# Optimization experiments

Measured on AMD Instinct MI355X. Metric: run time of the kernel, lower is better.

Reference implementation:

```python
import jax, jax.numpy as jnp
import numpy as np

NEG_SLOPE = 0.2

def setup_inputs() -> dict:
    key = jax.random.key(0)
    k1, k2, k3 = jax.random.split(key, 3)
    N, d, attn = 1024, 256, 256
    H = jax.random.normal(k1, (N, d), dtype=jnp.float32)
    # nn.Linear(2*d, attn, bias=False).weight has shape [attn, 2*d]
    W = jax.random.normal(k2, (attn, 2 * d), dtype=jnp.float32) * 0.05
    a = jax.random.normal(k3, (attn, 1), dtype=jnp.float32) * 0.05
    return {"H": H, "W": W, "a": a}

def reference(H, W, a):
    # Faithful to: E = leakyrelu(Linear(cat[H_i, H_j])); scores = E @ a; alpha = softmax(scores, dim=1); out = alpha @ H
    # Decompose W into halves acting on H_i and H_j to avoid the N x N x 2d concat:
    d = H.shape[1]
    W1, W2 = W[:, :d], W[:, d:]          # each [attn, d]
    Wh1 = H @ W1.T                        # [N, attn] (contribution of H_i)
    Wh2 = H @ W2.T                        # [N, attn] (contribution of H_j)
    E = jax.nn.leaky_relu(Wh1[:, None, :] + Wh2[None, :, :], NEG_SLOPE)  # [N, N, attn]
    scores = jnp.einsum('ijk,ko->ij', E, a)   # [N, N]
    alpha = jax.nn.softmax(scores, axis=1)    # softmax over j (dim=1)
    return alpha @ H                          # [N, d] weighted sum of H_j
```

## Files before the change

kernel.cpp:

```cpp
#include <hip/hip_runtime.h>


#define HALF 524288

#define FENCE_BAR() do {                                   \
    __builtin_amdgcn_sched_barrier(0);                     \
    asm volatile("s_waitcnt lgkmcnt(0)" ::: "memory");     \
    __builtin_amdgcn_s_barrier();                          \
    __builtin_amdgcn_sched_barrier(0);                     \
} while (0)

__global__ __launch_bounds__(256) void k1_gemm_wh(const float* __restrict__ H,
                                                  const float* __restrict__ W,
                                                  float* __restrict__ Whp) {
    __shared__ float As[64][36];
    __shared__ float Bs[32][36];
    const int bi = blockIdx.x, bm = blockIdx.y, bz = blockIdx.z;
    const int t = threadIdx.x;
    const int ti = t >> 4, tj = t & 15;
    const int i0 = ti * 4;
    const int half = bm >> 3;
    const int kbase = bz * 128;
    float acc[4][2] = {};
    for (int kc = 0; kc < 128; kc += 32) {
        const int kg = kbase + kc;
        {
            const int r = t >> 2, c = (t & 3) * 8;
            *(float4*)&As[r][c] = *(const float4*)&H[(bi * 64 + r) * 256 + kg + c];
            *(float4*)&As[r][c + 4] =
                *(const float4*)&H[(bi * 64 + r) * 256 + kg + c + 4];
        }
        {
            const int r = t >> 3, c = (t & 7) * 4;
            const int wrow = (bm * 32 + r) & 255;
            *(float4*)&Bs[r][c] =
                *(const float4*)&W[wrow * 512 + half * 256 + kg + c];
        }
        __syncthreads();
#pragma unroll
        for (int k = 0; k < 32; k += 4) {
            float4 a[4], b[2];
#pragma unroll
            for (int r = 0; r < 4; ++r) a[r] = *(const float4*)&As[i0 + r][k];
#pragma unroll
            for (int c = 0; c < 2; ++c) b[c] = *(const float4*)&Bs[tj + 16 * c][k];
#pragma unroll
            for (int r = 0; r < 4; ++r)
#pragma unroll
                for (int c = 0; c < 2; ++c) {
                    acc[r][c] = fmaf(a[r].x, b[c].x, acc[r][c]);
                    acc[r][c] = fmaf(a[r].y, b[c].y, acc[r][c]);
                    acc[r][c] = fmaf(a[r].z, b[c].z, acc[r][c]);
                    acc[r][c] = fmaf(a[r].w, b[c].w, acc[r][c]);
                }
        }
        __syncthreads();
    }
    float* dst = Whp + (size_t)bz * HALF;
#pragma unroll
    for (int r = 0; r < 4; ++r)
#pragma unroll
        for (int c = 0; c < 2; ++c)
            dst[(size_t)(bi * 64 + i0 + r) * 512 + bm * 32 + tj + 16 * c] = acc[r][c];
}

__global__ __launch_bounds__(256) void kW_merge(const float* __restrict__ Whp,
                                                const float* __restrict__ a,
                                                float* __restrict__ Wh,
                                                float* __restrict__ s2) {
    const int t = threadIdx.x;
    const int row = blockIdx.x * 2 + (t >> 7);
    const int col = (t & 127) * 4;
    const size_t off = (size_t)row * 512 + col;
    float4 v0 = *(const float4*)&Whp[off];
    float4 v1 = *(const float4*)&Whp[HALF + off];
    float4 v = make_float4(v0.x + v1.x, v0.y + v1.y, v0.z + v1.z, v0.w + v1.w);
    *(float4*)&Wh[off] = v;
    if (col >= 256) {
        float4 av = *(const float4*)&a[col - 256];
        float p = av.x * v.x + av.y * v.y + av.z * v.z + av.w * v.w;
#pragma unroll
        for (int o = 32; o > 0; o >>= 1) p += __shfl_xor(p, o);
        if ((t & 63) == 0) s2[row] = 0.6f * p;
    }
}

__global__ __launch_bounds__(256) void kF_flash(const float* __restrict__ Wh,
                                                const float* __restrict__ a,
                                                const float* __restrict__ s2,
                                                const float* __restrict__ H,
                                                float* __restrict__ avp,
                                                float* __restrict__ mbuf,
                                                float* __restrict__ lbuf) {
    __shared__ float SH[16640];
    __shared__ float P[32 * 68];
    __shared__ float bsh[256];
    float* X1 = SH;
    float* X2 = SH + 4352;
    float* Hs = SH;
    const int bi = blockIdx.x, bj = blockIdx.y;
    const int t = threadIdx.x;
    const int ti = t >> 4, tj = t & 15;
    const int i0 = ti * 2;
    const int r1 = t >> 3, c1 = (t & 7) * 8;
    const int r2 = t >> 2, c2 = (t & 3) * 16;
    const float* g1 = Wh + (size_t)(bi * 32 + r1) * 512 + c1;
    const float* g2 = Wh + (size_t)(bj * 64 + r2) * 512 + 256 + c2;
    const int hr = t >> 2, hc = (t & 3) * 64;
    const float* gH = H + (size_t)(bj * 64 + hr) * 256 + hc;

    float4 A0, A1, A2, A3, A4, A5, B0, B1, B2, B3, B4, B5;

#define LOADC_A(mc) do { A0 = *(const float4*)(g1 + (mc)*64); \
    A1 = *(const float4*)(g1 + (mc)*64 + 4);                  \
    A2 = *(const float4*)(g2 + (mc)*64);                      \
    A3 = *(const float4*)(g2 + (mc)*64 + 4);                  \
    A4 = *(const float4*)(g2 + (mc)*64 + 8);                  \
    A5 = *(const float4*)(g2 + (mc)*64 + 12); } while (0)
#define LOADC_B(mc) do { B0 = *(const float4*)(g1 + (mc)*64); \
    B1 = *(const float4*)(g1 + (mc)*64 + 4);                  \
    B2 = *(const float4*)(g2 + (mc)*64);                      \
    B3 = *(const float4*)(g2 + (mc)*64 + 4);                  \
    B4 = *(const float4*)(g2 + (mc)*64 + 8);                  \
    B5 = *(const float4*)(g2 + (mc)*64 + 12); } while (0)
#define WRITEC_A(buf) do {                                    \
    *(float4*)&X1[((buf) * 32 + r1) * 68 + c1] = A0;          \
    *(float4*)&X1[((buf) * 32 + r1) * 68 + c1 + 4] = A1;      \
    *(float4*)&X2[((buf) * 64 + r2) * 68 + c2] = A2;          \
    *(float4*)&X2[((buf) * 64 + r2) * 68 + c2 + 4] = A3;      \
    *(float4*)&X2[((buf) * 64 + r2) * 68 + c2 + 8] = A4;      \
    *(float4*)&X2[((buf) * 64 + r2) * 68 + c2 + 12] = A5; } while (0)
#define WRITEC_B(buf) do {                                    \
    *(float4*)&X1[((buf) * 32 + r1) * 68 + c1] = B0;          \
    *(float4*)&X1[((buf) * 32 + r1) * 68 + c1 + 4] = B1;      \
    *(float4*)&X2[((buf) * 64 + r2) * 68 + c2] = B2;          \
    *(float4*)&X2[((buf) * 64 + r2) * 68 + c2 + 4] = B3;      \
    *(float4*)&X2[((buf) * 64 + r2) * 68 + c2 + 8] = B4;      \
    *(float4*)&X2[((buf) * 64 + r2) * 68 + c2 + 12] = B5; } while (0)

    LOADC_A(0);
    float s2v0 = s2[bj * 64 + tj];
    float s2v1 = s2[bj * 64 + tj + 16];
    float s2v2 = s2[bj * 64 + tj + 32];
    float s2v3 = s2[bj * 64 + tj + 48];
    if (t < 64) {
        float4 av = *(const float4*)&a[t * 4];
        *(float4*)&bsh[t * 4] =
            make_float4(0.4f * av.x, 0.4f * av.y, 0.4f * av.z, 0.4f * av.w);
    }

    float acc[2][4] = {};
#pragma unroll
    for (int mc = 0; mc < 4; ++mc) {
        const int buf = mc & 1;
        if (mc < 3) {
            if (buf == 0) LOADC_B(mc + 1); else LOADC_A(mc + 1);
        }
        if (buf == 0) WRITEC_A(0); else WRITEC_B(1);
        FENCE_BAR();
#pragma unroll
        for (int k = 0; k < 64; k += 4) {
            float4 x1[2], x2[4];
#pragma unroll
            for (int r = 0; r < 2; ++r)
                x1[r] = *(const float4*)&X1[(buf * 32 + i0 + r) * 68 + k];
#pragma unroll
            for (int c = 0; c < 4; ++c)
                x2[c] = *(const float4*)&X2[(buf * 64 + tj + 16 * c) * 68 + k];
            const float4 bv = *(const float4*)&bsh[mc * 64 + k];
#pragma unroll
            for (int r = 0; r < 2; ++r)
#pragma unroll
                for (int c = 0; c < 4; ++c) {
                    acc[r][c] = fmaf(fabsf(x1[r].x + x2[c].x), bv.x, acc[r][c]);
                    acc[r][c] = fmaf(fabsf(x1[r].y + x2[c].y), bv.y, acc[r][c]);
                    acc[r][c] = fmaf(fabsf(x1[r].z + x2[c].z), bv.z, acc[r][c]);
                    acc[r][c] = fmaf(fabsf(x1[r].w + x2[c].w), bv.w, acc[r][c]);
                }
        }
        FENCE_BAR();
    }

    acc[0][0] += s2v0; acc[1][0] += s2v0;
    acc[0][1] += s2v1; acc[1][1] += s2v1;
    acc[0][2] += s2v2; acc[1][2] += s2v2;
    acc[0][3] += s2v3; acc[1][3] += s2v3;

    float4 h0 = *(const float4*)(gH);
    float4 h1 = *(const float4*)(gH + 4);
    float4 h2 = *(const float4*)(gH + 8);
    float4 h3 = *(const float4*)(gH + 12);
    float4 h4 = *(const float4*)(gH + 16);
    float4 h5 = *(const float4*)(gH + 20);
    float4 h6 = *(const float4*)(gH + 24);
    float4 h7 = *(const float4*)(gH + 28);

    float mm0, mm1, l00, l01;
#pragma unroll
    for (int r = 0; r < 2; ++r) {
        float mm = fmaxf(fmaxf(acc[r][0], acc[r][1]), fmaxf(acc[r][2], acc[r][3]));
        mm = fmaxf(mm, __shfl_xor(mm, 1));
        mm = fmaxf(mm, __shfl_xor(mm, 2));
        mm = fmaxf(mm, __shfl_xor(mm, 4));
        mm = fmaxf(mm, __shfl_xor(mm, 8));
        float l0 = 0.f;
#pragma unroll
        for (int c = 0; c < 4; ++c) {
            acc[r][c] = __expf(acc[r][c] - mm);
            l0 += acc[r][c];
        }
        l0 += __shfl_xor(l0, 1);
        l0 += __shfl_xor(l0, 2);
        l0 += __shfl_xor(l0, 4);
        l0 += __shfl_xor(l0, 8);
#pragma unroll
        for (int c = 0; c < 4; ++c) P[(i0 + r) * 68 + tj + 16 * c] = acc[r][c];
        if (r == 0) { mm0 = mm; l00 = l0; } else { mm1 = mm; l01 = l0; }
    }
    FENCE_BAR();

    *(float4*)&Hs[hr * 260 + hc] = h0;
    *(float4*)&Hs[hr * 260 + hc + 4] = h1;
    *(float4*)&Hs[hr * 260 + hc + 8] = h2;
    *(float4*)&Hs[hr * 260 + hc + 12] = h3;
    *(float4*)&Hs[hr * 260 + hc + 16] = h4;
    *(float4*)&Hs[hr * 260 + hc + 20] = h5;
    *(float4*)&Hs[hr * 260 + hc + 24] = h6;
    *(float4*)&Hs[hr * 260 + hc + 28] = h7;
    h0 = *(const float4*)(gH + 32);
    h1 = *(const float4*)(gH + 36);
    h2 = *(const float4*)(gH + 40);
    h3 = *(const float4*)(gH + 44);
    h4 = *(const float4*)(gH + 48);
    h5 = *(const float4*)(gH + 52);
    h6 = *(const float4*)(gH + 56);
    h7 = *(const float4*)(gH + 60);
    *(float4*)&Hs[hr * 260 + hc + 32] = h0;
    *(float4*)&Hs[hr * 260 + hc + 36] = h1;
    *(float4*)&Hs[hr * 260 + hc + 40] = h2;
    *(float4*)&Hs[hr * 260 + hc + 44] = h3;
    *(float4*)&Hs[hr * 260 + hc + 48] = h4;
    *(float4*)&Hs[hr * 260 + hc + 52] = h5;
    *(float4*)&Hs[hr * 260 + hc + 56] = h6;
    *(float4*)&Hs[hr * 260 + hc + 60] = h7;
    FENCE_BAR();

    const int ti2 = t >> 5, tj2 = t & 31;
    const int ip = ti2 * 4;
    const int ca = tj2 * 4, cb = 128 + tj2 * 4;
    float4 acc2[4][2] = {};
#pragma unroll
    for (int jj = 0; jj < 64; jj += 4) {
        float4 pv[4];
#pragma unroll
        for (int r = 0; r < 4; ++r) pv[r] = *(const float4*)&P[(ip + r) * 68 + jj];
#pragma unroll
        for (int q = 0; q < 4; ++q) {
            float4 ha = *(const float4*)&Hs[(jj + q) * 260 + ca];
            float4 hb = *(const float4*)&Hs[(jj + q) * 260 + cb];
#pragma unroll
            for (int r = 0; r < 4; ++r) {
                const float s = (q == 0) ? pv[r].x : (q == 1) ? pv[r].y
                              : (q == 2) ? pv[r].z : pv[r].w;
                acc2[r][0].x = fmaf(s, ha.x, acc2[r][0].x);
                acc2[r][0].y = fmaf(s, ha.y, acc2[r][0].y);
                acc2[r][0].z = fmaf(s, ha.z, acc2[r][0].z);
                acc2[r][0].w = fmaf(s, ha.w, acc2[r][0].w);
                acc2[r][1].x = fmaf(s, hb.x, acc2[r][1].x);
                acc2[r][1].y = fmaf(s, hb.y, acc2[r][1].y);
                acc2[r][1].z = fmaf(s, hb.z, acc2[r][1].z);
                acc2[r][1].w = fmaf(s, hb.w, acc2[r][1].w);
            }
        }
    }
#pragma unroll
    for (int r = 0; r < 4; ++r) {
        const size_t o = (size_t)bj * 262144 + (size_t)(bi * 32 + ip + r) * 256;
        *(float4*)&avp[o + ca] = acc2[r][0];
        *(float4*)&avp[o + cb] = acc2[r][1];
    }
    if (tj == 0) {
        const int gi = bi * 32 + i0;
        mbuf[bj * 1024 + gi] = mm0;
        lbuf[bj * 1024 + gi] = l00;
        mbuf[bj * 1024 + gi + 1] = mm1;
        lbuf[bj * 1024 + gi + 1] = l01;
    }
#undef LOADC_A
#undef LOADC_B
#undef WRITEC_A
#undef WRITEC_B
}

__global__ __launch_bounds__(256) void kM_merge(const float* __restrict__ avp,
                                                const float* __restrict__ mbuf,
                                                const float* __restrict__ lbuf,
                                                float* __restrict__ out) {
    const int t = threadIdx.x;
    const int i = blockIdx.x * 4 + (t >> 6);
    const int c0 = (t & 63) * 4;
    float ms[16], es[16];
    float M = -1e30f;
#pragma unroll
    for (int s = 0; s < 16; ++s) {
        ms[s] = mbuf[s * 1024 + i];
        M = fmaxf(M, ms[s]);
    }
    float L = 0.f;
#pragma unroll
    for (int s = 0; s < 16; ++s) {
        es[s] = __expf(ms[s] - M);
        L = fmaf(es[s], lbuf[s * 1024 + i], L);
    }
    const float inv = 1.0f / L;
    float4 o = make_float4(0.f, 0.f, 0.f, 0.f);
#pragma unroll
    for (int s = 0; s < 16; ++s) {
        float4 p = *(const float4*)&avp[(size_t)s * 262144 + (size_t)i * 256 + c0];
        o.x = fmaf(es[s], p.x, o.x);
        o.y = fmaf(es[s], p.y, o.y);
        o.z = fmaf(es[s], p.z, o.z);
        o.w = fmaf(es[s], p.w, o.w);
    }
    o.x *= inv; o.y *= inv; o.z *= inv; o.w *= inv;
    *(float4*)&out[(size_t)i * 256 + c0] = o;
}

extern "C" void kernel_launch(void* const* d_in, const int* in_sizes, int n_in,
                              void* d_out, int out_size, void* d_ws, size_t ws_size,
                              hipStream_t stream) {
    const float* H = (const float*)d_in[0];
    const float* W = (const float*)d_in[1];
    const float* a = (const float*)d_in[2];
    float* out = (float*)d_out;
    float* ws = (float*)d_ws;

    float* avp = ws;
    float* Whp = ws;
    float* Wh = ws + (4u << 20);
    float* mbuf = Wh + HALF;
    float* lbuf = mbuf + 16384;
    float* s2 = lbuf + 16384;

    hipLaunchKernelGGL(k1_gemm_wh, dim3(16, 16, 2), dim3(256), 0, stream, H, W, Whp);
    hipLaunchKernelGGL(kW_merge, dim3(512), dim3(256), 0, stream, Whp, a, Wh, s2);
    hipLaunchKernelGGL(kF_flash, dim3(32, 16), dim3(256), 0, stream, Wh, a, s2, H,
                       avp, mbuf, lbuf);
    hipLaunchKernelGGL(kM_merge, dim3(256), dim3(256), 0, stream, avp, mbuf, lbuf, out);
}
```

Measured before the change: 49.29 us.

## Halve flash block size, double per-thread tile, prefetch two chunks ahead

The flash kernel now runs 128 threads per block instead of 256 over the same 32x64 tile, so each thread computes 4x4 scores and 8 output rows of the P@H product. Register-staged loads of Wh chunks move to a prefetch-two-ahead scheme. The pre-scaled attention vector is written to global memory once by the merge kernel rather than rebuilt in shared memory by every block. The aim is more register-level reuse per LDS load and less per-block overhead, at the cost of higher register pressure (h[32], acc2[8][2], A/B[12]), which could spill or cut occupancy.

```diff
diff --git a/kernel.cpp b/kernel.cpp
--- a/kernel.cpp
+++ b/kernel.cpp
@@ -9,6 +9,13 @@
     __builtin_amdgcn_s_barrier();                          \
     __builtin_amdgcn_sched_barrier(0);                     \
 } while (0)
+
+__device__ __forceinline__ void f4fma(float4& acc, float s, float4 h) {
+    acc.x = fmaf(s, h.x, acc.x);
+    acc.y = fmaf(s, h.y, acc.y);
+    acc.z = fmaf(s, h.z, acc.z);
+    acc.w = fmaf(s, h.w, acc.w);
+}
 
 __global__ __launch_bounds__(256) void k1_gemm_wh(const float* __restrict__ H,
                                                   const float* __restrict__ W,
@@ -67,7 +74,8 @@
 __global__ __launch_bounds__(256) void kW_merge(const float* __restrict__ Whp,
                                                 const float* __restrict__ a,
                                                 float* __restrict__ Wh,
-                                                float* __restrict__ s2) {
+                                                float* __restrict__ s2,
+                                                float* __restrict__ bglob) {
     const int t = threadIdx.x;
     const int row = blockIdx.x * 2 + (t >> 7);
     const int col = (t & 127) * 4;
@@ -83,93 +91,93 @@
         for (int o = 32; o > 0; o >>= 1) p += __shfl_xor(p, o);
         if ((t & 63) == 0) s2[row] = 0.6f * p;
     }
-}
-
-__global__ __launch_bounds__(256) void kF_flash(const float* __restrict__ Wh,
-                                                const float* __restrict__ a,
+    if (blockIdx.x == 0 && t < 64) {
+        float4 av = *(const float4*)&a[t * 4];
+        *(float4*)&bglob[t * 4] =
+            make_float4(0.4f * av.x, 0.4f * av.y, 0.4f * av.z, 0.4f * av.w);
+    }
+}
+
+__global__ __launch_bounds__(128) void kF_flash(const float* __restrict__ Wh,
+                                                const float* __restrict__ bglob,
                                                 const float* __restrict__ s2,
                                                 const float* __restrict__ H,
                                                 float* __restrict__ avp,
                                                 float* __restrict__ mbuf,
                                                 float* __restrict__ lbuf) {
     __shared__ float SH[16640];
-    __shared__ float P[32 * 68];
-    __shared__ float bsh[256];
+    __shared__ float P[2176];
     float* X1 = SH;
     float* X2 = SH + 4352;
     float* Hs = SH;
     const int bi = blockIdx.x, bj = blockIdx.y;
     const int t = threadIdx.x;
     const int ti = t >> 4, tj = t & 15;
-    const int i0 = ti * 2;
-    const int r1 = t >> 3, c1 = (t & 7) * 8;
-    const int r2 = t >> 2, c2 = (t & 3) * 16;
+    const int i0 = ti * 4;
+    const int r1 = t >> 2, c1 = (t & 3) * 16;
+    const int r2 = t >> 1, c2 = (t & 1) * 32;
     const float* g1 = Wh + (size_t)(bi * 32 + r1) * 512 + c1;
     const float* g2 = Wh + (size_t)(bj * 64 + r2) * 512 + 256 + c2;
-    const int hr = t >> 2, hc = (t & 3) * 64;
-    const float* gH = H + (size_t)(bj * 64 + hr) * 256 + hc;
-
-    float4 A0, A1, A2, A3, A4, A5, B0, B1, B2, B3, B4, B5;
-
-#define LOADC_A(mc) do { A0 = *(const float4*)(g1 + (mc)*64); \
-    A1 = *(const float4*)(g1 + (mc)*64 + 4);                  \
-    A2 = *(const float4*)(g2 + (mc)*64);                      \
-    A3 = *(const float4*)(g2 + (mc)*64 + 4);                  \
-    A4 = *(const float4*)(g2 + (mc)*64 + 8);                  \
-    A5 = *(const float4*)(g2 + (mc)*64 + 12); } while (0)
-#define LOADC_B(mc) do { B0 = *(const float4*)(g1 + (mc)*64); \
-    B1 = *(const float4*)(g1 + (mc)*64 + 4);                  \
-    B2 = *(const float4*)(g2 + (mc)*64);                      \
-    B3 = *(const float4*)(g2 + (mc)*64 + 4);                  \
-    B4 = *(const float4*)(g2 + (mc)*64 + 8);                  \
-    B5 = *(const float4*)(g2 + (mc)*64 + 12); } while (0)
-#define WRITEC_A(buf) do {                                    \
-    *(float4*)&X1[((buf) * 32 + r1) * 68 + c1] = A0;          \
-    *(float4*)&X1[((buf) * 32 + r1) * 68 + c1 + 4] = A1;      \
-    *(float4*)&X2[((buf) * 64 + r2) * 68 + c2] = A2;          \
-    *(float4*)&X2[((buf) * 64 + r2) * 68 + c2 + 4] = A3;      \
-    *(float4*)&X2[((buf) * 64 + r2) * 68 + c2 + 8] = A4;      \
-    *(float4*)&X2[((buf) * 64 + r2) * 68 + c2 + 12] = A5; } while (0)
-#define WRITEC_B(buf) do {                                    \
-    *(float4*)&X1[((buf) * 32 + r1) * 68 + c1] = B0;          \
-    *(float4*)&X1[((buf) * 32 + r1) * 68 + c1 + 4] = B1;      \
-    *(float4*)&X2[((buf) * 64 + r2) * 68 + c2] = B2;          \
-    *(float4*)&X2[((buf) * 64 + r2) * 68 + c2 + 4] = B3;      \
-    *(float4*)&X2[((buf) * 64 + r2) * 68 + c2 + 8] = B4;      \
-    *(float4*)&X2[((buf) * 64 + r2) * 68 + c2 + 12] = B5; } while (0)
-
-    LOADC_A(0);
+    const int hr = t & 63, hcb = (t >> 6) * 128;
+    const float* gH = H + (size_t)(bj * 64 + hr) * 256 + hcb;
+
+    float4 A[12], B[12];
+
+#define LOADC(R, mc) do {                                       \
+    R[0] = *(const float4*)(g1 + (mc) * 64);                    \
+    R[1] = *(const float4*)(g1 + (mc) * 64 + 4);                \
+    R[2] = *(const float4*)(g1 + (mc) * 64 + 8);                \
+    R[3] = *(const float4*)(g1 + (mc) * 64 + 12);               \
+    R[4] = *(const float4*)(g2 + (mc) * 64);                    \
+    R[5] = *(const float4*)(g2 + (mc) * 64 + 4);                \
+    R[6] = *(const float4*)(g2 + (mc) * 64 + 8);                \
+    R[7] = *(const float4*)(g2 + (mc) * 64 + 12);               \
+    R[8] = *(const float4*)(g2 + (mc) * 64 + 16);               \
+    R[9] = *(const float4*)(g2 + (mc) * 64 + 20);               \
+    R[10] = *(const float4*)(g2 + (mc) * 64 + 24);              \
+    R[11] = *(const float4*)(g2 + (mc) * 64 + 28); } while (0)
+#define WRITEC(R, buf) do {                                     \
+    *(float4*)&X1[((buf) * 32 + r1) * 68 + c1] = R[0];          \
+    *(float4*)&X1[((buf) * 32 + r1) * 68 + c1 + 4] = R[1];      \
+    *(float4*)&X1[((buf) * 32 + r1) * 68 + c1 + 8] = R[2];      \
+    *(float4*)&X1[((buf) * 32 + r1) * 68 + c1 + 12] = R[3];     \
+    *(float4*)&X2[((buf) * 64 + r2) * 68 + c2] = R[4];          \
+    *(float4*)&X2[((buf) * 64 + r2) * 68 + c2 + 4] = R[5];      \
+    *(float4*)&X2[((buf) * 64 + r2) * 68 + c2 + 8] = R[6];      \
+    *(float4*)&X2[((buf) * 64 + r2) * 68 + c2 + 12] = R[7];     \
+    *(float4*)&X2[((buf) * 64 + r2) * 68 + c2 + 16] = R[8];     \
+    *(float4*)&X2[((buf) * 64 + r2) * 68 + c2 + 20] = R[9];     \
+    *(float4*)&X2[((buf) * 64 + r2) * 68 + c2 + 24] = R[10];    \
+    *(float4*)&X2[((buf) * 64 + r2) * 68 + c2 + 28] = R[11]; } while (0)
+
+    LOADC(A, 0);
+    LOADC(B, 1);
     float s2v0 = s2[bj * 64 + tj];
     float s2v1 = s2[bj * 64 + tj + 16];
     float s2v2 = s2[bj * 64 + tj + 32];
     float s2v3 = s2[bj * 64 + tj + 48];
-    if (t < 64) {
-        float4 av = *(const float4*)&a[t * 4];
-        *(float4*)&bsh[t * 4] =
-            make_float4(0.4f * av.x, 0.4f * av.y, 0.4f * av.z, 0.4f * av.w);
-    }
-
-    float acc[2][4] = {};
+    WRITEC(A, 0);
+    FENCE_BAR();
+
+    float acc[4][4] = {};
 #pragma unroll
     for (int mc = 0; mc < 4; ++mc) {
         const int buf = mc & 1;
-        if (mc < 3) {
-            if (buf == 0) LOADC_B(mc + 1); else LOADC_A(mc + 1);
-        }
-        if (buf == 0) WRITEC_A(0); else WRITEC_B(1);
-        FENCE_BAR();
+        if (mc == 0) { WRITEC(B, 1); LOADC(A, 2); }
+        else if (mc == 1) { WRITEC(A, 0); LOADC(B, 3); }
+        else if (mc == 2) { WRITEC(B, 1); }
 #pragma unroll
         for (int k = 0; k < 64; k += 4) {
-            float4 x1[2], x2[4];
-#pragma unroll
-            for (int r = 0; r < 2; ++r)
+            float4 x1[4], x2[4];
+#pragma unroll
+            for (int r = 0; r < 4; ++r)
                 x1[r] = *(const float4*)&X1[(buf * 32 + i0 + r) * 68 + k];
 #pragma unroll
             for (int c = 0; c < 4; ++c)
                 x2[c] = *(const float4*)&X2[(buf * 64 + tj + 16 * c) * 68 + k];
-            const float4 bv = *(const float4*)&bsh[mc * 64 + k];
-#pragma unroll
-            for (int r = 0; r < 2; ++r)
+            const float4 bv = *(const float4*)(bglob + mc * 64 + k);
+#pragma unroll
+            for (int r = 0; r < 4; ++r)
 #pragma unroll
                 for (int c = 0; c < 4; ++c) {
                     acc[r][c] = fmaf(fabsf(x1[r].x + x2[c].x), bv.x, acc[r][c]);
@@ -181,23 +189,19 @@
         FENCE_BAR();
     }
 
-    acc[0][0] += s2v0; acc[1][0] += s2v0;
-    acc[0][1] += s2v1; acc[1][1] += s2v1;
-    acc[0][2] += s2v2; acc[1][2] += s2v2;
-    acc[0][3] += s2v3; acc[1][3] += s2v3;
-
-    float4 h0 = *(const float4*)(gH);
-    float4 h1 = *(const float4*)(gH + 4);
-    float4 h2 = *(const float4*)(gH + 8);
-    float4 h3 = *(const float4*)(gH + 12);
-    float4 h4 = *(const float4*)(gH + 16);
-    float4 h5 = *(const float4*)(gH + 20);
-    float4 h6 = *(const float4*)(gH + 24);
-    float4 h7 = *(const float4*)(gH + 28);
-
-    float mm0, mm1, l00, l01;
-#pragma unroll
-    for (int r = 0; r < 2; ++r) {
+#pragma unroll
+    for (int r = 0; r < 4; ++r) {
+        acc[r][0] += s2v0; acc[r][1] += s2v1;
+        acc[r][2] += s2v2; acc[r][3] += s2v3;
+    }
+
+    float4 h[32];
+#pragma unroll
+    for (int q = 0; q < 32; ++q) h[q] = *(const float4*)(gH + q * 4);
+
+    float mmv[4], llv[4];
+#pragma unroll
+    for (int r = 0; r < 4; ++r) {
         float mm = fmaxf(fmaxf(acc[r][0], acc[r][1]), fmaxf(acc[r][2], acc[r][3]));
         mm = fmaxf(mm, __shfl_xor(mm, 1));
         mm = fmaxf(mm, __shfl_xor(mm, 2));
@@ -215,81 +219,52 @@
         l0 += __shfl_xor(l0, 8);
 #pragma unroll
         for (int c = 0; c < 4; ++c) P[(i0 + r) * 68 + tj + 16 * c] = acc[r][c];
-        if (r == 0) { mm0 = mm; l00 = l0; } else { mm1 = mm; l01 = l0; }
+        mmv[r] = mm; llv[r] = l0;
     }
     FENCE_BAR();
 
-    *(float4*)&Hs[hr * 260 + hc] = h0;
-    *(float4*)&Hs[hr * 260 + hc + 4] = h1;
-    *(float4*)&Hs[hr * 260 + hc + 8] = h2;
-    *(float4*)&Hs[hr * 260 + hc + 12] = h3;
-    *(float4*)&Hs[hr * 260 + hc + 16] = h4;
-    *(float4*)&Hs[hr * 260 + hc + 20] = h5;
-    *(float4*)&Hs[hr * 260 + hc + 24] = h6;
-    *(float4*)&Hs[hr * 260 + hc + 28] = h7;
-    h0 = *(const float4*)(gH + 32);
-    h1 = *(const float4*)(gH + 36);
-    h2 = *(const float4*)(gH + 40);
-    h3 = *(const float4*)(gH + 44);
-    h4 = *(const float4*)(gH + 48);
-    h5 = *(const float4*)(gH + 52);
-    h6 = *(const float4*)(gH + 56);
-    h7 = *(const float4*)(gH + 60);
-    *(float4*)&Hs[hr * 260 + hc + 32] = h0;
-    *(float4*)&Hs[hr * 260 + hc + 36] = h1;
-    *(float4*)&Hs[hr * 260 + hc + 40] = h2;
-    *(float4*)&Hs[hr * 260 + hc + 44] = h3;
-    *(float4*)&Hs[hr * 260 + hc + 48] = h4;
-    *(float4*)&Hs[hr * 260 + hc + 52] = h5;
-    *(float4*)&Hs[hr * 260 + hc + 56] = h6;
-    *(float4*)&Hs[hr * 260 + hc + 60] = h7;
+#pragma unroll
+    for (int q = 0; q < 32; ++q) *(float4*)&Hs[hr * 260 + hcb + q * 4] = h[q];
     FENCE_BAR();
 
     const int ti2 = t >> 5, tj2 = t & 31;
-    const int ip = ti2 * 4;
+    const int ip = ti2 * 8;
     const int ca = tj2 * 4, cb = 128 + tj2 * 4;
-    float4 acc2[4][2] = {};
+    float4 acc2[8][2] = {};
 #pragma unroll
     for (int jj = 0; jj < 64; jj += 4) {
-        float4 pv[4];
-#pragma unroll
-        for (int r = 0; r < 4; ++r) pv[r] = *(const float4*)&P[(ip + r) * 68 + jj];
+        float4 pv[8];
+#pragma unroll
+        for (int r = 0; r < 8; ++r) pv[r] = *(const float4*)&P[(ip + r) * 68 + jj];
 #pragma unroll
         for (int q = 0; q < 4; ++q) {
             float4 ha = *(const float4*)&Hs[(jj + q) * 260 + ca];
             float4 hb = *(const float4*)&Hs[(jj + q) * 260 + cb];
 #pragma unroll
-            for (int r = 0; r < 4; ++r) {
+            for (int r = 0; r < 8; ++r) {
                 const float s = (q == 0) ? pv[r].x : (q == 1) ? pv[r].y
                               : (q == 2) ? pv[r].z : pv[r].w;
-                acc2[r][0].x = fmaf(s, ha.x, acc2[r][0].x);
-                acc2[r][0].y = fmaf(s, ha.y, acc2[r][0].y);
-                acc2[r][0].z = fmaf(s, ha.z, acc2[r][0].z);
-                acc2[r][0].w = fmaf(s, ha.w, acc2[r][0].w);
-                acc2[r][1].x = fmaf(s, hb.x, acc2[r][1].x);
-                acc2[r][1].y = fmaf(s, hb.y, acc2[r][1].y);
-                acc2[r][1].z = fmaf(s, hb.z, acc2[r][1].z);
-                acc2[r][1].w = fmaf(s, hb.w, acc2[r][1].w);
+                f4fma(acc2[r][0], s, ha);
+                f4fma(acc2[r][1], s, hb);
             }
         }
     }
 #pragma unroll
-    for (int r = 0; r < 4; ++r) {
+    for (int r = 0; r < 8; ++r) {
         const size_t o = (size_t)bj * 262144 + (size_t)(bi * 32 + ip + r) * 256;
         *(float4*)&avp[o + ca] = acc2[r][0];
         *(float4*)&avp[o + cb] = acc2[r][1];
     }
     if (tj == 0) {
         const int gi = bi * 32 + i0;
-        mbuf[bj * 1024 + gi] = mm0;
-        lbuf[bj * 1024 + gi] = l00;
-        mbuf[bj * 1024 + gi + 1] = mm1;
-        lbuf[bj * 1024 + gi + 1] = l01;
-    }
-#undef LOADC_A
-#undef LOADC_B
-#undef WRITEC_A
-#undef WRITEC_B
+#pragma unroll
+        for (int r = 0; r < 4; ++r) {
+            mbuf[bj * 1024 + gi + r] = mmv[r];
+            lbuf[bj * 1024 + gi + r] = llv[r];
+        }
+    }
+#undef LOADC
+#undef WRITEC
 }
 
 __global__ __launch_bounds__(256) void kM_merge(const float* __restrict__ avp,
@@ -341,10 +316,11 @@
     float* mbuf = Wh + HALF;
     float* lbuf = mbuf + 16384;
     float* s2 = lbuf + 16384;
+    float* bglob = s2 + 1024;
 
     hipLaunchKernelGGL(k1_gemm_wh, dim3(16, 16, 2), dim3(256), 0, stream, H, W, Whp);
-    hipLaunchKernelGGL(kW_merge, dim3(512), dim3(256), 0, stream, Whp, a, Wh, s2);
-    hipLaunchKernelGGL(kF_flash, dim3(32, 16), dim3(256), 0, stream, Wh, a, s2, H,
+    hipLaunchKernelGGL(kW_merge, dim3(512), dim3(256), 0, stream, Whp, a, Wh, s2, bglob);
+    hipLaunchKernelGGL(kF_flash, dim3(32, 16), dim3(128), 0, stream, Wh, bglob, s2, H,
                        avp, mbuf, lbuf);
     hipLaunchKernelGGL(kM_merge, dim3(256), dim3(256), 0, stream, avp, mbuf, lbuf, out);
 }
```

After: 71.23 us. 44.5% more time.
